# Performance work log

Measured on AMD Instinct MI355X. Metric: run time of the kernel, lower is better.

## Reference

```python
import jax, jax.numpy as jnp
import numpy as np

KERNEL_MUL = 2.0
KERNEL_NUM = 5


def _index_matrix(b: int) -> jnp.ndarray:
    # non-linear JMMD index matrix (linear=False)
    im = np.zeros((2 * b, 2 * b), dtype=np.float32)
    off = 1.0 / float(b * (b - 1))
    eye = np.eye(b, dtype=bool)
    im[:b, :b][~eye] = off
    im[b:, b:][~eye] = off
    im[:b, b:] = -1.0 / float(b * b)
    im[b:, :b] = -1.0 / float(b * b)
    return jnp.asarray(im)


def _gaussian_kernel(source, target):
    total = jnp.concatenate([source, target], axis=0)  # [2b, d]
    n = total.shape[0]
    sq = jnp.sum(total * total, axis=1)  # [2b]
    # pairwise squared L2 via Gram matrix (same math as expand/diff/sum)
    l2 = sq[:, None] + sq[None, :] - 2.0 * (total @ total.T)
    l2 = jnp.maximum(l2, 0.0)
    # bandwidth computed on detached distances (torch uses .data)
    bw = jax.lax.stop_gradient(jnp.sum(l2)) / float(n * n - n)
    bw = bw / (KERNEL_MUL ** (KERNEL_NUM // 2))
    k = jnp.zeros_like(l2)
    for i in range(KERNEL_NUM):
        k = k + jnp.exp(-l2 / (bw * (KERNEL_MUL ** i)))
    return k


def setup_inputs() -> dict:
    key = jax.random.key(0)
    k1, k2, k3, k4 = jax.random.split(key, 4)
    b, d1, d2 = 2048, 4096, 2048
    return {
        "z1_s": jax.random.normal(k1, (b, d1), dtype=jnp.float32),
        "z1_t": jax.random.normal(k2, (b, d1), dtype=jnp.float32),
        "z2_s": jax.random.normal(k3, (b, d2), dtype=jnp.float32),
        "z2_t": jax.random.normal(k4, (b, d2), dtype=jnp.float32),
    }


def reference(z1_s, z1_t, z2_s, z2_t):
    b = z1_s.shape[0]
    index_matrix = _index_matrix(b)  # [2b, 2b]
    kernel_matrix = _gaussian_kernel(z1_s, z1_t) * _gaussian_kernel(z2_s, z2_t)
    loss = jnp.sum(kernel_matrix * index_matrix) + 2.0 / float(b - 1)
    return loss
```

## Files before the change

kernel.cpp:

```cpp
#include <hip/hip_runtime.h>
#include <cstdint>

#define NTOT 4096
#define BHALF 2048
#define D1 4096
#define D2 2048
#define TT 32
#define NTILES 528

typedef __attribute__((ext_vector_type(4))) float f32x4;
typedef __attribute__((ext_vector_type(4))) int i32x4;
typedef __attribute__((ext_vector_type(8))) int i32x8;

__device__ __forceinline__ void glds16(const uint8_t* g, uint8_t* l) {
    __builtin_amdgcn_global_load_lds(
        (const __attribute__((address_space(1))) void*)(uintptr_t)g,
        (__attribute__((address_space(3))) void*)(uint32_t)(uintptr_t)l,
        16, 0, 0);
}

__device__ __forceinline__ i32x4 ldsr(uint32_t addr) {
    i32x4 r;
    asm volatile("ds_read_b128 %0, %1" : "=v"(r) : "v"(addr));
    return r;
}

__device__ __forceinline__ float fp8dec(unsigned b) {
    unsigned e = (b >> 3) & 15u, m = b & 7u;
    float v = e ? __uint_as_float(((e + 120u) << 23) | (m << 20))
                : (float)m * 0.001953125f;
    return (b & 128u) ? -v : v;
}

__global__ void prep_kernel(const float* __restrict__ z1s, const float* __restrict__ z1t,
                            const float* __restrict__ z2s, const float* __restrict__ z2t,
                            float* __restrict__ sq1, float* __restrict__ sq2,
                            uint8_t* __restrict__ t1f8, uint8_t* __restrict__ t2f8,
                            float* __restrict__ s1, float* __restrict__ s2) {
    int bid = blockIdx.x;
    int tid = threadIdx.x;
    if (bid == 0) { for (int i = tid; i < 4096; i += 256) s1[i] = 0.f; }
    if (bid == 1) { for (int i = tid; i < 2048; i += 256) s2[i] = 0.f; }
    int which = bid >> 12;
    int row = bid & 4095;
    int d = which ? D2 : D1;
    const float* s_ = which ? z2s : z1s;
    const float* t_ = which ? z2t : z1t;
    const float* src = (row < BHALF) ? s_ + (size_t)row * d : t_ + (size_t)(row - BHALF) * d;
    uint8_t* dst = (which ? t2f8 : t1f8) + (size_t)row * d;
    float* sq = which ? sq2 : sq1;
    const float4* src4 = (const float4*)src;
    float a = 0.f;
    int n8 = d >> 3;
    for (int i = tid; i < n8; i += 256) {
        float4 v0 = src4[2 * i], v1 = src4[2 * i + 1];
        a += v0.x * v0.x + v0.y * v0.y + v0.z * v0.z + v0.w * v0.w;
        a += v1.x * v1.x + v1.y * v1.y + v1.z * v1.z + v1.w * v1.w;
        int w0 = __builtin_amdgcn_cvt_pk_fp8_f32(v0.x, v0.y, 0, 0);
        w0 = __builtin_amdgcn_cvt_pk_fp8_f32(v0.z, v0.w, w0, 1);
        int w1 = __builtin_amdgcn_cvt_pk_fp8_f32(v1.x, v1.y, 0, 0);
        w1 = __builtin_amdgcn_cvt_pk_fp8_f32(v1.z, v1.w, w1, 1);
        ((uint2*)dst)[i] = uint2{(unsigned)w0, (unsigned)w1};
    }
    for (int o = 32; o; o >>= 1) a += __shfl_down(a, o);
    __shared__ float sh[4];
    int lane = tid & 63, w = tid >> 6;
    if (lane == 0) sh[w] = a;
    __syncthreads();
    if (tid == 0) sq[row] = sh[0] + sh[1] + sh[2] + sh[3];
}

__global__ void colsum_fp8_kernel(const uint8_t* __restrict__ t1f8,
                                  const uint8_t* __restrict__ t2f8,
                                  float* __restrict__ s1, float* __restrict__ s2) {
    int bid = blockIdx.x;
    int which = bid >= 256;
    int local = which ? bid - 256 : bid;
    int d = which ? D2 : D1;
    int colchunks = d >> 10;
    int cb = local % colchunks, rb = local / colchunks;
    const uint8_t* base = which ? t2f8 : t1f8;
    float* s = which ? s2 : s1;
    int col = (cb << 10) + threadIdx.x * 4;
    int r0 = rb * 64;
    float a0 = 0.f, a1 = 0.f, a2 = 0.f, a3 = 0.f;
    const uint8_t* p = base + (size_t)r0 * d + col;
#pragma unroll 4
    for (int r = 0; r < 64; ++r) {
        uchar4 u = *(const uchar4*)(p + (size_t)r * d);
        a0 += fp8dec(u.x); a1 += fp8dec(u.y); a2 += fp8dec(u.z); a3 += fp8dec(u.w);
    }
    atomicAdd(&s[col], a0); atomicAdd(&s[col + 1], a1);
    atomicAdd(&s[col + 2], a2); atomicAdd(&s[col + 3], a3);
}

__global__ void finalize_kernel(const float* __restrict__ s1, const float* __restrict__ s2,
                                const float* __restrict__ sq1, const float* __restrict__ sq2,
                                float* __restrict__ acc, float* __restrict__ out) {
    int tid = threadIdx.x;
    float a1 = 0.f, a2 = 0.f, q1 = 0.f, q2 = 0.f;
    for (int i = tid; i < 4096; i += 256) { float v = s1[i]; a1 += v * v; q1 += sq1[i]; q2 += sq2[i]; }
    for (int i = tid; i < 2048; i += 256) { float v = s2[i]; a2 += v * v; }
    for (int o = 32; o; o >>= 1) {
        a1 += __shfl_down(a1, o); a2 += __shfl_down(a2, o);
        q1 += __shfl_down(q1, o); q2 += __shfl_down(q2, o);
    }
    __shared__ float sh[4][4];
    int lane = tid & 63, w = tid >> 6;
    if (lane == 0) { sh[0][w] = a1; sh[1][w] = a2; sh[2][w] = q1; sh[3][w] = q2; }
    __syncthreads();
    if (tid == 0) {
        double ss1 = (double)sh[0][0] + sh[0][1] + sh[0][2] + sh[0][3];
        double ss2 = (double)sh[1][0] + sh[1][1] + sh[1][2] + sh[1][3];
        double t1 = (double)sh[2][0] + sh[2][1] + sh[2][2] + sh[2][3];
        double t2 = (double)sh[3][0] + sh[3][1] + sh[3][2] + sh[3][3];
        double S1 = 2.0 * (double)NTOT * t1 - 2.0 * ss1;
        double S2 = 2.0 * (double)NTOT * t2 - 2.0 * ss2;
        const double L2E = 1.4426950408889634;
        double nn = (double)NTOT * (double)(NTOT - 1);
        acc[2] = (float)(nn * L2E / (4.0 * S1));
        acc[3] = (float)(nn * L2E / (4.0 * S2));
        out[0] = 2.0f / (float)(BHALF - 1);
    }
}

__device__ __forceinline__ void gemm_mx_pipe(const uint8_t* __restrict__ ga,
                                             const uint8_t* __restrict__ gb,
                                             int d,
                                             uint8_t* A0, uint8_t* B0,
                                             uint8_t* A1, uint8_t* B1,
                                             f32x4 (&acc)[4][4], int wv, int lane,
                                             int wm, int wn, int lm, int quad) {
    int nsteps = d >> 7;
    int rsub = lane >> 3;
    int ql = (lane & 7) ^ rsub;
    const uint8_t* pa = ga + (size_t)(wv * 32 + rsub) * d + ql * 16;
    const uint8_t* pb = gb + (size_t)(wv * 32 + rsub) * d + ql * 16;
    uint8_t* dA[2] = { A0 + wv * 4096, A1 + wv * 4096 };
    uint8_t* dB[2] = { B0 + wv * 4096, B1 + wv * 4096 };
    uint32_t baseA[2] = { (uint32_t)(uintptr_t)A0, (uint32_t)(uintptr_t)A1 };
    uint32_t baseB[2] = { (uint32_t)(uintptr_t)B0, (uint32_t)(uintptr_t)B1 };
    int s0 = ((2 * quad) ^ (lm & 7)) * 16;
    int s1 = ((2 * quad + 1) ^ (lm & 7)) * 16;
    uint32_t offA[4], offB[4];
#pragma unroll
    for (int i = 0; i < 4; ++i) {
        offA[i] = (uint32_t)((wm * 64 + i * 16 + lm) * 128);
        offB[i] = (uint32_t)((wn * 64 + i * 16 + lm) * 128);
    }
#pragma unroll
    for (int i = 0; i < 4; ++i) {
        glds16(pa + (size_t)i * 8 * d, dA[0] + i * 1024);
        glds16(pb + (size_t)i * 8 * d, dB[0] + i * 1024);
    }
    for (int k = 0; k < nsteps; ++k) {
        int cur = k & 1, nxt = cur ^ 1;
        size_t koff = (size_t)((k + 1 < nsteps) ? (k + 1) : 0) << 7;
#pragma unroll
        for (int i = 0; i < 4; ++i) {
            glds16(pa + koff + (size_t)i * 8 * d, dA[nxt] + i * 1024);
            glds16(pb + koff + (size_t)i * 8 * d, dB[nxt] + i * 1024);
        }
        asm volatile("s_waitcnt vmcnt(8)\n\ts_barrier" ::: "memory");
        i32x4 a00, a01, a10, a11, a20, a21, a30, a31;
        i32x4 b00, b01, b10, b11, b20, b21, b30, b31;
        a00 = ldsr(baseA[cur] + offA[0] + s0); a01 = ldsr(baseA[cur] + offA[0] + s1);
        a10 = ldsr(baseA[cur] + offA[1] + s0); a11 = ldsr(baseA[cur] + offA[1] + s1);
        a20 = ldsr(baseA[cur] + offA[2] + s0); a21 = ldsr(baseA[cur] + offA[2] + s1);
        a30 = ldsr(baseA[cur] + offA[3] + s0); a31 = ldsr(baseA[cur] + offA[3] + s1);
        b00 = ldsr(baseB[cur] + offB[0] + s0); b01 = ldsr(baseB[cur] + offB[0] + s1);
        b10 = ldsr(baseB[cur] + offB[1] + s0); b11 = ldsr(baseB[cur] + offB[1] + s1);
        b20 = ldsr(baseB[cur] + offB[2] + s0); b21 = ldsr(baseB[cur] + offB[2] + s1);
        b30 = ldsr(baseB[cur] + offB[3] + s0); b31 = ldsr(baseB[cur] + offB[3] + s1);
        asm volatile("s_waitcnt lgkmcnt(0)"
                     : "+v"(a00), "+v"(a01), "+v"(a10), "+v"(a11),
                       "+v"(a20), "+v"(a21), "+v"(a30), "+v"(a31),
                       "+v"(b00), "+v"(b01), "+v"(b10), "+v"(b11),
                       "+v"(b20), "+v"(b21), "+v"(b30), "+v"(b31));
        union F { i32x4 h[2]; i32x8 v; };
        F ua[4], ub[4];
        ua[0].h[0] = a00; ua[0].h[1] = a01; ua[1].h[0] = a10; ua[1].h[1] = a11;
        ua[2].h[0] = a20; ua[2].h[1] = a21; ua[3].h[0] = a30; ua[3].h[1] = a31;
        ub[0].h[0] = b00; ub[0].h[1] = b01; ub[1].h[0] = b10; ub[1].h[1] = b11;
        ub[2].h[0] = b20; ub[2].h[1] = b21; ub[3].h[0] = b30; ub[3].h[1] = b31;
#pragma unroll
        for (int ni = 0; ni < 4; ++ni)
#pragma unroll
            for (int mi = 0; mi < 4; ++mi)
                acc[mi][ni] = __builtin_amdgcn_mfma_scale_f32_16x16x128_f8f6f4(
                    ua[mi].v, ub[ni].v, acc[mi][ni], 0, 0, 0, 0x7F7F7F7F, 0, 0x7F7F7F7F);
        asm volatile("s_barrier" ::: "memory");
    }
}

__global__ __launch_bounds__(256, 2) void gram_kernel(
    const uint8_t* __restrict__ t1f8, const uint8_t* __restrict__ t2f8,
    float* __restrict__ G1, float* __restrict__ G2) {
    __shared__ alignas(16) uint8_t smem[4][16384];
    int lid = blockIdx.x;
    int lin = (lid & 7) * 132 + (lid >> 3);
    int ti, tj, which;
    if (lin < 768) {
        int r = lin >> 7, q = lin & 127;
        which = q & 1;
        int t = q >> 1, a = t >> 3, b = t & 7;
        const int si_t[6] = {0, 0, 0, 1, 1, 2};
        const int sj_t[6] = {1, 2, 3, 2, 3, 3};
        ti = si_t[r] * 8 + a; tj = sj_t[r] * 8 + b;
    } else {
        int m = lin - 768;
        int dd = m / 144, q = m % 144;
        which = q & 1;
        int t = q >> 1;
        int s = 2 * dd + (t >= 36 ? 1 : 0);
        int tl = t >= 36 ? t - 36 : t;
        int a = 0;
        while (tl >= 8 - a) { tl -= 8 - a; ++a; }
        ti = s * 8 + a; tj = s * 8 + a + tl;
    }
    int tcan = TT * ti - (ti * (ti - 1)) / 2 + (tj - ti);
    int i0 = ti * 128, j0 = tj * 128;
    int d = which ? D2 : D1;
    const uint8_t* base = which ? t2f8 : t1f8;
    float* G = (which ? G2 : G1) + (size_t)tcan * 16384;

    int tid = threadIdx.x, lane = tid & 63, wv = tid >> 6;
    int wm = wv >> 1, wn = wv & 1, lm = lane & 15, quad = lane >> 4;
    f32x4 acc[4][4] = {};
    gemm_mx_pipe(base + (size_t)i0 * d, base + (size_t)j0 * d, d,
                 smem[0], smem[1], smem[2], smem[3],
                 acc, wv, lane, wm, wn, lm, quad);
#pragma unroll
    for (int mi = 0; mi < 4; ++mi)
#pragma unroll
        for (int ni = 0; ni < 4; ++ni)
#pragma unroll
            for (int rr = 0; rr < 4; ++rr)
                G[(size_t)(wm * 64 + mi * 16 + quad * 4 + rr) * 128 + wn * 64 + ni * 16 + lm] =
                    acc[mi][ni][rr];
}

__global__ __launch_bounds__(256, 4) void epi_kernel(
    const float* __restrict__ G1, const float* __restrict__ G2,
    const float* __restrict__ sq1, const float* __restrict__ sq2,
    const float* __restrict__ cv, float* __restrict__ out) {
    __shared__ float sqi1[128], sqj1[128], sqi2[128], sqj2[128];
    __shared__ float red[4];
    int t = blockIdx.x;
    int ti = 0, r = t;
    while (r >= TT - ti) { r -= TT - ti; ++ti; }
    int tj = ti + r;
    int i0 = ti * 128, j0 = tj * 128;
    int tid = threadIdx.x;
    if (tid < 128) {
        sqi1[tid] = sq1[i0 + tid]; sqj1[tid] = sq1[j0 + tid];
        sqi2[tid] = sq2[i0 + tid]; sqj2[tid] = sq2[j0 + tid];
    }
    __syncthreads();
    float c1 = cv[0], c2 = cv[1];
    const float4* g1 = (const float4*)(G1 + (size_t)t * 16384);
    const float4* g2 = (const float4*)(G2 + (size_t)t * 16384);
    bool diag = (ti == tj);
    float local = 0.f;
#pragma unroll 4
    for (int it = 0; it < 16; ++it) {
        int e4 = it * 256 + tid;
        int row = e4 >> 5, col = (e4 & 31) * 4;
        float4 a = g1[e4], b = g2[e4];
        float si1 = sqi1[row], si2 = sqi2[row];
        float ax[4] = {a.x, a.y, a.z, a.w}, bx[4] = {b.x, b.y, b.z, b.w};
#pragma unroll
        for (int j = 0; j < 4; ++j) {
            float l2a = fmaxf(si1 + sqj1[col + j] - 2.f * ax[j], 0.f);
            float l2b = fmaxf(si2 + sqj2[col + j] - 2.f * bx[j], 0.f);
            float t1 = __builtin_amdgcn_exp2f(-l2a * c1);
            float k1 = t1; float u1 = t1 * t1; k1 += u1; u1 *= u1; k1 += u1; u1 *= u1; k1 += u1; u1 *= u1; k1 += u1;
            float t2 = __builtin_amdgcn_exp2f(-l2b * c2);
            float k2 = t2; float u2 = t2 * t2; k2 += u2; u2 *= u2; k2 += u2; u2 *= u2; k2 += u2; u2 *= u2; k2 += u2;
            float v = k1 * k2;
            if (diag && (row == col + j)) v = 0.f;
            local += v;
        }
    }
    for (int o = 32; o; o >>= 1) local += __shfl_down(local, o);
    int lane = tid & 63, wv = tid >> 6;
    if (lane == 0) red[wv] = local;
    __syncthreads();
    if (tid == 0) {
        bool same = (i0 < BHALF) == (j0 < BHALF);
        float w = same ? (1.0f / ((float)BHALF * (float)(BHALF - 1)))
                       : (-1.0f / ((float)BHALF * (float)BHALF));
        if (!diag) w *= 2.f;
        atomicAdd(out, (red[0] + red[1] + red[2] + red[3]) * w);
    }
}

__global__ __launch_bounds__(256, 2) void jmmd_fused(
    const uint8_t* __restrict__ t1f8, const uint8_t* __restrict__ t2f8,
    const float* __restrict__ sq1, const float* __restrict__ sq2,
    const float* __restrict__ cv, float* __restrict__ out) {
    __shared__ alignas(16) uint8_t smem[4][16384];
    __shared__ float sqi1[128], sqj1[128], sqi2[128], sqj2[128];
    __shared__ float red[4];
    int tid = threadIdx.x;
    int ti = 0, r = blockIdx.x;
    while (r >= TT - ti) { r -= TT - ti; ++ti; }
    int tj = ti + r;
    int i0 = ti * 128, j0 = tj * 128;
    if (tid < 128) {
        sqi1[tid] = sq1[i0 + tid]; sqj1[tid] = sq1[j0 + tid];
        sqi2[tid] = sq2[i0 + tid]; sqj2[tid] = sq2[j0 + tid];
    }
    int lane = tid & 63, wv = tid >> 6;
    int wm = wv >> 1, wn = wv & 1, lm = lane & 15, quad = lane >> 4;
    f32x4 acc1[4][4] = {};
    f32x4 acc2[4][4] = {};
    gemm_mx_pipe(t1f8 + (size_t)i0 * D1, t1f8 + (size_t)j0 * D1, D1,
                 smem[0], smem[1], smem[2], smem[3], acc1, wv, lane, wm, wn, lm, quad);
    asm volatile("s_waitcnt vmcnt(0)\n\ts_barrier" ::: "memory");
    gemm_mx_pipe(t2f8 + (size_t)i0 * D2, t2f8 + (size_t)j0 * D2, D2,
                 smem[0], smem[1], smem[2], smem[3], acc2, wv, lane, wm, wn, lm, quad);
    float c1 = cv[0], c2 = cv[1];
    float local = 0.f;
    bool diag = (ti == tj);
#pragma unroll
    for (int mi = 0; mi < 4; ++mi) {
        int rbase = wm * 64 + mi * 16 + quad * 4;
#pragma unroll
        for (int ni = 0; ni < 4; ++ni) {
            int col = wn * 64 + ni * 16 + lm;
            float sb1 = sqj1[col], sb2 = sqj2[col];
#pragma unroll
            for (int rr = 0; rr < 4; ++rr) {
                int row = rbase + rr;
                float l2a = fmaxf(sqi1[row] + sb1 - 2.f * acc1[mi][ni][rr], 0.f);
                float l2b = fmaxf(sqi2[row] + sb2 - 2.f * acc2[mi][ni][rr], 0.f);
                float t1 = __builtin_amdgcn_exp2f(-l2a * c1);
                float k1 = t1; float u1 = t1 * t1; k1 += u1; u1 *= u1; k1 += u1; u1 *= u1; k1 += u1; u1 *= u1; k1 += u1;
                float t2 = __builtin_amdgcn_exp2f(-l2b * c2);
                float k2 = t2; float u2 = t2 * t2; k2 += u2; u2 *= u2; k2 += u2; u2 *= u2; k2 += u2; u2 *= u2; k2 += u2;
                float v = k1 * k2;
                if (diag && (row == col)) v = 0.f;
                local += v;
            }
        }
    }
    for (int o = 32; o; o >>= 1) local += __shfl_down(local, o);
    if (lane == 0) red[wv] = local;
    __syncthreads();
    if (tid == 0) {
        bool same = (i0 < BHALF) == (j0 < BHALF);
        float w = same ? (1.0f / ((float)BHALF * (float)(BHALF - 1)))
                       : (-1.0f / ((float)BHALF * (float)BHALF));
        if (!diag) w *= 2.f;
        atomicAdd(out, (red[0] + red[1] + red[2] + red[3]) * w);
    }
}

extern "C" void kernel_launch(void* const* d_in, const int* in_sizes, int n_in,
                              void* d_out, int out_size, void* d_ws, size_t ws_size,
                              hipStream_t stream) {
    const float* z1s = (const float*)d_in[0];
    const float* z1t = (const float*)d_in[1];
    const float* z2s = (const float*)d_in[2];
    const float* z2t = (const float*)d_in[3];
    float* out = (float*)d_out;

    float* ws = (float*)d_ws;
    float* sq1 = ws;
    float* sq2 = ws + 4096;
    float* s1  = ws + 8192;
    float* s2  = ws + 12288;
    float* acc = ws + 14336;
    uint8_t* t1f8 = (uint8_t*)(ws + 14344);
    uint8_t* t2f8 = t1f8 + (size_t)NTOT * D1;
    float* G1 = (float*)(t2f8 + (size_t)NTOT * D2);
    float* G2 = G1 + (size_t)NTILES * 16384;
    size_t need_big = (size_t)14344 * 4
                    + ((size_t)NTOT * D1 + (size_t)NTOT * D2)
                    + (size_t)NTILES * 16384 * 2 * 4;

    prep_kernel<<<8192, 256, 0, stream>>>(z1s, z1t, z2s, z2t, sq1, sq2, t1f8, t2f8, s1, s2);
    colsum_fp8_kernel<<<384, 256, 0, stream>>>(t1f8, t2f8, s1, s2);
    finalize_kernel<<<1, 256, 0, stream>>>(s1, s2, sq1, sq2, acc, out);

    if (ws_size >= need_big) {
        gram_kernel<<<1056, 256, 0, stream>>>(t1f8, t2f8, G1, G2);
        epi_kernel<<<NTILES, 256, 0, stream>>>(G1, G2, sq1, sq2, acc + 2, out);
    } else {
        jmmd_fused<<<NTILES, 256, 0, stream>>>(t1f8, t2f8, sq1, sq2, acc + 2, out);
    }
}
```

Before: 294.4 us.

## Always use fused gram+epilogue kernel instead of split gram/epilogue path

Removes the two-kernel path that wrote both fp32 Gram tile sets to workspace and then reread them for the Gaussian-kernel epilogue. The single fused kernel computes both Gram tiles per block and applies the exp/sum epilogue in registers, which avoids roughly 70 MB of global writes and reads and one launch. The trade-off is only 528 blocks, each doing both GEMMs serially, against 1056 independently scheduled blocks, so there is less parallelism and load balance across the GPU.

```diff
diff --git a/kernel.cpp b/kernel.cpp
--- a/kernel.cpp
+++ b/kernel.cpp
@@ -193,108 +193,6 @@
     }
 }
 
-__global__ __launch_bounds__(256, 2) void gram_kernel(
-    const uint8_t* __restrict__ t1f8, const uint8_t* __restrict__ t2f8,
-    float* __restrict__ G1, float* __restrict__ G2) {
-    __shared__ alignas(16) uint8_t smem[4][16384];
-    int lid = blockIdx.x;
-    int lin = (lid & 7) * 132 + (lid >> 3);
-    int ti, tj, which;
-    if (lin < 768) {
-        int r = lin >> 7, q = lin & 127;
-        which = q & 1;
-        int t = q >> 1, a = t >> 3, b = t & 7;
-        const int si_t[6] = {0, 0, 0, 1, 1, 2};
-        const int sj_t[6] = {1, 2, 3, 2, 3, 3};
-        ti = si_t[r] * 8 + a; tj = sj_t[r] * 8 + b;
-    } else {
-        int m = lin - 768;
-        int dd = m / 144, q = m % 144;
-        which = q & 1;
-        int t = q >> 1;
-        int s = 2 * dd + (t >= 36 ? 1 : 0);
-        int tl = t >= 36 ? t - 36 : t;
-        int a = 0;
-        while (tl >= 8 - a) { tl -= 8 - a; ++a; }
-        ti = s * 8 + a; tj = s * 8 + a + tl;
-    }
-    int tcan = TT * ti - (ti * (ti - 1)) / 2 + (tj - ti);
-    int i0 = ti * 128, j0 = tj * 128;
-    int d = which ? D2 : D1;
-    const uint8_t* base = which ? t2f8 : t1f8;
-    float* G = (which ? G2 : G1) + (size_t)tcan * 16384;
-
-    int tid = threadIdx.x, lane = tid & 63, wv = tid >> 6;
-    int wm = wv >> 1, wn = wv & 1, lm = lane & 15, quad = lane >> 4;
-    f32x4 acc[4][4] = {};
-    gemm_mx_pipe(base + (size_t)i0 * d, base + (size_t)j0 * d, d,
-                 smem[0], smem[1], smem[2], smem[3],
-                 acc, wv, lane, wm, wn, lm, quad);
-#pragma unroll
-    for (int mi = 0; mi < 4; ++mi)
-#pragma unroll
-        for (int ni = 0; ni < 4; ++ni)
-#pragma unroll
-            for (int rr = 0; rr < 4; ++rr)
-                G[(size_t)(wm * 64 + mi * 16 + quad * 4 + rr) * 128 + wn * 64 + ni * 16 + lm] =
-                    acc[mi][ni][rr];
-}
-
-__global__ __launch_bounds__(256, 4) void epi_kernel(
-    const float* __restrict__ G1, const float* __restrict__ G2,
-    const float* __restrict__ sq1, const float* __restrict__ sq2,
-    const float* __restrict__ cv, float* __restrict__ out) {
-    __shared__ float sqi1[128], sqj1[128], sqi2[128], sqj2[128];
-    __shared__ float red[4];
-    int t = blockIdx.x;
-    int ti = 0, r = t;
-    while (r >= TT - ti) { r -= TT - ti; ++ti; }
-    int tj = ti + r;
-    int i0 = ti * 128, j0 = tj * 128;
-    int tid = threadIdx.x;
-    if (tid < 128) {
-        sqi1[tid] = sq1[i0 + tid]; sqj1[tid] = sq1[j0 + tid];
-        sqi2[tid] = sq2[i0 + tid]; sqj2[tid] = sq2[j0 + tid];
-    }
-    __syncthreads();
-    float c1 = cv[0], c2 = cv[1];
-    const float4* g1 = (const float4*)(G1 + (size_t)t * 16384);
-    const float4* g2 = (const float4*)(G2 + (size_t)t * 16384);
-    bool diag = (ti == tj);
-    float local = 0.f;
-#pragma unroll 4
-    for (int it = 0; it < 16; ++it) {
-        int e4 = it * 256 + tid;
-        int row = e4 >> 5, col = (e4 & 31) * 4;
-        float4 a = g1[e4], b = g2[e4];
-        float si1 = sqi1[row], si2 = sqi2[row];
-        float ax[4] = {a.x, a.y, a.z, a.w}, bx[4] = {b.x, b.y, b.z, b.w};
-#pragma unroll
-        for (int j = 0; j < 4; ++j) {
-            float l2a = fmaxf(si1 + sqj1[col + j] - 2.f * ax[j], 0.f);
-            float l2b = fmaxf(si2 + sqj2[col + j] - 2.f * bx[j], 0.f);
-            float t1 = __builtin_amdgcn_exp2f(-l2a * c1);
-            float k1 = t1; float u1 = t1 * t1; k1 += u1; u1 *= u1; k1 += u1; u1 *= u1; k1 += u1; u1 *= u1; k1 += u1;
-            float t2 = __builtin_amdgcn_exp2f(-l2b * c2);
-            float k2 = t2; float u2 = t2 * t2; k2 += u2; u2 *= u2; k2 += u2; u2 *= u2; k2 += u2; u2 *= u2; k2 += u2;
-            float v = k1 * k2;
-            if (diag && (row == col + j)) v = 0.f;
-            local += v;
-        }
-    }
-    for (int o = 32; o; o >>= 1) local += __shfl_down(local, o);
-    int lane = tid & 63, wv = tid >> 6;
-    if (lane == 0) red[wv] = local;
-    __syncthreads();
-    if (tid == 0) {
-        bool same = (i0 < BHALF) == (j0 < BHALF);
-        float w = same ? (1.0f / ((float)BHALF * (float)(BHALF - 1)))
-                       : (-1.0f / ((float)BHALF * (float)BHALF));
-        if (!diag) w *= 2.f;
-        atomicAdd(out, (red[0] + red[1] + red[2] + red[3]) * w);
-    }
-}
-
 __global__ __launch_bounds__(256, 2) void jmmd_fused(
     const uint8_t* __restrict__ t1f8, const uint8_t* __restrict__ t2f8,
     const float* __restrict__ sq1, const float* __restrict__ sq2,
@@ -374,20 +272,9 @@
     float* acc = ws + 14336;
     uint8_t* t1f8 = (uint8_t*)(ws + 14344);
     uint8_t* t2f8 = t1f8 + (size_t)NTOT * D1;
-    float* G1 = (float*)(t2f8 + (size_t)NTOT * D2);
-    float* G2 = G1 + (size_t)NTILES * 16384;
-    size_t need_big = (size_t)14344 * 4
-                    + ((size_t)NTOT * D1 + (size_t)NTOT * D2)
-                    + (size_t)NTILES * 16384 * 2 * 4;
 
     prep_kernel<<<8192, 256, 0, stream>>>(z1s, z1t, z2s, z2t, sq1, sq2, t1f8, t2f8, s1, s2);
     colsum_fp8_kernel<<<384, 256, 0, stream>>>(t1f8, t2f8, s1, s2);
     finalize_kernel<<<1, 256, 0, stream>>>(s1, s2, sq1, sq2, acc, out);
-
-    if (ws_size >= need_big) {
-        gram_kernel<<<1056, 256, 0, stream>>>(t1f8, t2f8, G1, G2);
-        epi_kernel<<<NTILES, 256, 0, stream>>>(G1, G2, sq1, sq2, acc + 2, out);
-    } else {
-        jmmd_fused<<<NTILES, 256, 0, stream>>>(t1f8, t2f8, sq1, sq2, acc + 2, out);
-    }
-}
+    jmmd_fused<<<NTILES, 256, 0, stream>>>(t1f8, t2f8, sq1, sq2, acc + 2, out);
+}
```

Measured after the change: 277.3 us. 5.8% less time.
